# Optimization experiments

Measured on AMD Instinct MI355X. Metric: run time of the kernel, lower is better.

Reference implementation:

```python
import jax, jax.numpy as jnp
import numpy as np
import math

DN = ('NCHW', 'OIHW', 'NCHW')

def conv(x, w, b, stride=1, pad=0):
    y = jax.lax.conv_general_dilated(x, w, (stride, stride), ((pad, pad), (pad, pad)), dimension_numbers=DN)
    return y + b[None, :, None, None]

def conv_t(x, w, b, stride=2, k=4, p=1):
    # torch ConvTranspose2d: weight (Cin, Cout, kH, kW). Equivalent fractionally-strided conv:
    w2 = jnp.transpose(w[:, :, ::-1, ::-1], (1, 0, 2, 3))  # -> (Cout, Cin, kH, kW), spatially flipped
    pp = k - 1 - p
    y = jax.lax.conv_general_dilated(x, w2, (1, 1), ((pp, pp), (pp, pp)), lhs_dilation=(stride, stride), dimension_numbers=DN)
    return y + b[None, :, None, None]

def res_stack(h, w1, b1, w2, b2):
    # w1: [L, rh, nh, 3, 3], w2: [L, nh, rh, 1, 1]
    for i in range(w1.shape[0]):
        t = conv(jax.nn.relu(h), w1[i], b1[i], 1, 1)
        t = conv(jax.nn.relu(t), w2[i], b2[i], 1, 0)
        h = h + t
    return jax.nn.relu(h)

def setup_inputs() -> dict:
    key = jax.random.key(0)
    ks = jax.random.split(key, 16)
    D, K = 64, 512
    limit = math.sqrt(3.0 / D)
    def w(k, shape, scale=0.05):
        return (jax.random.normal(k, shape, dtype=jnp.float32) * scale)
    return {
        'x': jax.random.normal(ks[0], (16, 3, 256, 256), dtype=jnp.float32),
        'enc_w0': w(ks[1], (64, 3, 4, 4)), 'enc_b0': jnp.zeros((64,), jnp.float32),
        'enc_w1': w(ks[2], (128, 64, 4, 4)), 'enc_b1': jnp.zeros((128,), jnp.float32),
        'enc_wf': w(ks[3], (128, 128, 3, 3)), 'enc_bf': jnp.zeros((128,), jnp.float32),
        'enc_res_w1': w(ks[4], (2, 32, 128, 3, 3)), 'enc_res_b1': jnp.zeros((2, 32), jnp.float32),
        'enc_res_w2': w(ks[5], (2, 128, 32, 1, 1)), 'enc_res_b2': jnp.zeros((2, 128), jnp.float32),
        'pre_w': w(ks[6], (64, 128, 1, 1)), 'pre_b': jnp.zeros((64,), jnp.float32),
        'codebook': jax.random.uniform(ks[7], (D, K), jnp.float32, -limit, limit),
        'dec_w': w(ks[8], (128, 64, 3, 3)), 'dec_b': jnp.zeros((128,), jnp.float32),
        'dec_res_w1': w(ks[9], (2, 32, 128, 3, 3)), 'dec_res_b1': jnp.zeros((2, 32), jnp.float32),
        'dec_res_w2': w(ks[10], (2, 128, 32, 1, 1)), 'dec_res_b2': jnp.zeros((2, 128), jnp.float32),
        'up_w0': w(ks[11], (128, 64, 4, 4)), 'up_b0': jnp.zeros((64,), jnp.float32),
        'up_w1': w(ks[12], (64, 3, 4, 4)), 'up_b1': jnp.zeros((3,), jnp.float32),
    }

def reference(x, enc_w0, enc_b0, enc_w1, enc_b1, enc_wf, enc_bf,
              enc_res_w1, enc_res_b1, enc_res_w2, enc_res_b2,
              pre_w, pre_b, codebook,
              dec_w, dec_b, dec_res_w1, dec_res_b1, dec_res_w2, dec_res_b2,
              up_w0, up_b0, up_w1, up_b1):
    # --- Encoder ---
    h = jax.nn.relu(conv(x, enc_w0, enc_b0, 2, 1))
    h = jax.nn.relu(conv(h, enc_w1, enc_b1, 2, 1))
    h = conv(h, enc_wf, enc_bf, 1, 1)
    h = res_stack(h, enc_res_w1, enc_res_b1, enc_res_w2, enc_res_b2)
    z = conv(h, pre_w, pre_b, 1, 0)  # [B, 64, 64, 64]
    # --- Vector quantizer (cdist + argmin + gather, straight-through) ---
    B, D, H, W = z.shape
    flat = jnp.transpose(z, (0, 2, 3, 1)).reshape(-1, D)  # [BHW, D]
    dist = (flat ** 2).sum(1, keepdims=True) - 2.0 * (flat @ codebook) + (codebook ** 2).sum(0)[None, :]
    idx = jnp.argmin(dist, axis=1)  # [BHW]
    q = codebook.T[idx].reshape(B, H, W, D).transpose(0, 3, 1, 2)
    zq = z + jax.lax.stop_gradient(q - z)  # straight-through estimator
    # --- Decoder ---
    h = conv(zq, dec_w, dec_b, 1, 1)
    h = res_stack(h, dec_res_w1, dec_res_b1, dec_res_w2, dec_res_b2)
    h = jax.nn.relu(conv_t(h, up_w0, up_b0, 2, 4, 1))
    x_recon = conv_t(h, up_w1, up_b1, 2, 4, 1)
    return x_recon
```

## Files before the change

### kernel.cpp

```cpp
#include <hip/hip_runtime.h>
#include <math.h>


#define DEV __device__ __forceinline__

DEV int rfl(int v) { return __builtin_amdgcn_readfirstlane(v); }

DEV void async_copy16(const float* g, float* l) {
  __builtin_amdgcn_global_load_lds(
      (const __attribute__((address_space(1))) void*)g,
      (__attribute__((address_space(3))) void*)l, 16, 0, 0);
}

typedef __attribute__((ext_vector_type(8))) _Float16 h16x8;
typedef __attribute__((ext_vector_type(4))) float f32x4;

DEV ushort f2h(float f) {
  _Float16 h = (_Float16)f;
  return __builtin_bit_cast(ushort, h);
}
DEV float h2f(ushort u) { return (float)__builtin_bit_cast(_Float16, u); }
DEV uint pk(ushort a, ushort b) { return (uint)a | ((uint)b << 16); }

template<int CIN, int COT>
__global__ __launch_bounds__(256) void prep_w3s(
    const float* __restrict__ w, ushort* __restrict__ wpk) {
  constexpr int nCh = CIN / 32, nM = COT / 16;
  const int t = blockIdx.x * 256 + threadIdx.x;
  if (t >= 9 * nCh * nM * 64) return;
  const int l = t & 63;
  const int m = (t >> 6) % nM;
  const int sid = t / (64 * nM);
  const int ch = sid / 9, khkw = sid % 9;
  const int co = m * 16 + (l & 15);
  const int k8 = (l >> 4) * 8;
  const int sw = (16 * l) ^ ((l & 4) ? 8 : 0);
  ushort* slab = wpk + (size_t)sid * (nM * 1024) + m * 1024;
#pragma unroll
  for (int i = 0; i < 8; i++) {
    const int ci = ch * 32 + k8 + i;
    const float v = w[((size_t)co * CIN + ci) * 9 + khkw];
    const ushort hi = f2h(v);
    slab[sw + i]       = hi;
    slab[(sw ^ 8) + i] = f2h((v - h2f(hi)) * 2048.0f);
  }
}

template<int CIN, int COT>
__global__ __launch_bounds__(256) void prep_w4s(
    const float* __restrict__ w, ushort* __restrict__ wpk) {
  const int t = blockIdx.x * 256 + threadIdx.x;
  if (t >= 16384) return;
  const int l = t & 63;
  const int m = (t >> 6) & 7;
  const int sid = t >> 9;
  const int step = sid >> 3, rr = (sid >> 2) & 1, kw = sid & 3;
  const int ch = step >> 1, h = step & 1;
  const int kh = 2 * h + rr;
  const int tap = kh * 4 + kw;
  const int co = m * 16 + (l & 15);
  const int k8 = (l >> 4) * 8;
  const int sw = (16 * l) ^ ((l & 4) ? 8 : 0);
  ushort* slab = wpk + (size_t)sid * 8192 + m * 1024;
#pragma unroll
  for (int i = 0; i < 8; i++) {
    const int ci = ch * 32 + k8 + i;
    const float v = w[((size_t)co * CIN + ci) * 16 + tap];
    const ushort hi = f2h(v);
    slab[sw + i]       = hi;
    slab[(sw ^ 8) + i] = f2h((v - h2f(hi)) * 2048.0f);
  }
}

template<int CIN, int COT>
__global__ __launch_bounds__(256) void prep_wts(
    const float* __restrict__ w, ushort* __restrict__ wpk) {
  constexpr int nCh = CIN / 32, nM = COT / 16;
  const int t = blockIdx.x * 256 + threadIdx.x;
  if (t >= 16 * nCh * nM * 64) return;
  const int l = t & 63;
  const int m = (t >> 6) % nM;
  const int sid = t / (64 * nM);
  const int ch = sid >> 4, idx = sid & 15;
  const int ord[16] = {15, 13, 14, 12, 7, 11, 5, 6, 9, 10, 4, 8, 3, 1, 2, 0};
  const int tap = ord[idx];
  const int kh = tap >> 2, kw = tap & 3;
  const int co = m * 16 + (l & 15);
  const int k8 = (l >> 4) * 8;
  const int sw = (16 * l) ^ ((l & 4) ? 8 : 0);
  ushort* slab = wpk + (size_t)sid * (nM * 1024) + m * 1024;
#pragma unroll
  for (int i = 0; i < 8; i++) {
    const int ci = ch * 32 + k8 + i;
    const float v = w[(((size_t)ci * COT + co) * 4 + kh) * 4 + kw];
    const ushort hi = f2h(v);
    slab[sw + i]       = hi;
    slab[(sw ^ 8) + i] = f2h((v - h2f(hi)) * 2048.0f);
  }
}

__global__ __launch_bounds__(256) void prep_cb(
    const float* __restrict__ cb, ushort* __restrict__ cbpk) {
  const int t = blockIdx.x * 256 + threadIdx.x;
  const int l = t & 63;
  const int m = (t >> 6) & 31;
  const int c = t >> 11;
  const int entry = m * 16 + (l & 15);
  ushort* o = cbpk + (size_t)t * 16;
#pragma unroll
  for (int i = 0; i < 8; i++) {
    const int d = c * 32 + (l >> 4) * 8 + i;
    const float v = cb[d * 512 + entry];
    const ushort hi = f2h(v);
    o[i]     = hi;
    o[8 + i] = f2h((v - h2f(hi)) * 2048.0f);
  }
}

__global__ __launch_bounds__(256) void cvt_cbn(
    const float* __restrict__ cb, float* __restrict__ cbn) {
  const int k = blockIdx.x * 256 + threadIdx.x;
  if (k >= 512) return;
  double s = 0.0;
  for (int d = 0; d < 64; d++) {
    const double c = (double)cb[d * 512 + k];
    s = fma(c, c, s);
  }
  cbn[k] = (float)s;
}

__global__ __launch_bounds__(256) void vq_mfma(
    const float* __restrict__ cb, const ushort* __restrict__ cbpk,
    const float* __restrict__ cbn, float* __restrict__ zq) {
  const int tid = threadIdx.x;
  const int l = tid & 63;
  const int w = rfl(tid >> 6);
  const int n = blockIdx.x >> 6, row = blockIdx.x & 63;
  float* zp = zq + (size_t)n * 262144 + row * 64;
  const int pos = w * 16 + (l & 15);

  h16x8 zh[2], zl[2];
#pragma unroll
  for (int c = 0; c < 2; c++) {
#pragma unroll
    for (int i = 0; i < 8; i++) {
      const int d = c * 32 + (l >> 4) * 8 + i;
      const float v = zp[(size_t)d * 4096 + pos];
      const _Float16 h = (_Float16)v;
      zh[c][i] = h;
      zl[c][i] = (_Float16)((v - (float)h) * 2048.0f);
    }
  }

  const float SCL = 1.0f / 2048.0f;
  float bestd = 1e30f;
  int best = 0;
  for (int grp = 0; grp < 4; grp++) {
    f32x4 aH[8], aM[8];
#pragma unroll
    for (int m = 0; m < 8; m++) {
      aH[m] = (f32x4){0.f, 0.f, 0.f, 0.f};
      aM[m] = (f32x4){0.f, 0.f, 0.f, 0.f};
    }
#pragma unroll
    for (int c = 0; c < 2; c++) {
#pragma unroll
      for (int m = 0; m < 8; m++) {
        const ushort* ap = cbpk + ((size_t)(c * 32 + grp * 8 + m) * 64 + l) * 16;
        const h16x8 ah = *(const h16x8*)ap;
        const h16x8 al = *(const h16x8*)(ap + 8);
        aH[m] = __builtin_amdgcn_mfma_f32_16x16x32_f16(ah, zh[c], aH[m], 0, 0, 0);
        aM[m] = __builtin_amdgcn_mfma_f32_16x16x32_f16(al, zh[c], aM[m], 0, 0, 0);
        aM[m] = __builtin_amdgcn_mfma_f32_16x16x32_f16(ah, zl[c], aM[m], 0, 0, 0);
      }
    }
#pragma unroll
    for (int m = 0; m < 8; m++) {
#pragma unroll
      for (int j = 0; j < 4; j++) {
        const int k = grp * 128 + m * 16 + ((l >> 4) << 2) + j;
        const float dd = aH[m][j] + aM[m][j] * SCL;
        const float dist = fmaf(-2.0f, dd, cbn[k]);
        if (dist < bestd) { bestd = dist; best = k; }
      }
    }
  }

#pragma unroll
  for (int off = 16; off <= 32; off <<= 1) {
    const float d2 = __shfl_xor(bestd, off, 64);
    const int i2 = __shfl_xor(best, off, 64);
    if (d2 < bestd || (d2 == bestd && i2 < best)) { bestd = d2; best = i2; }
  }

#pragma unroll
  for (int i = 0; i < 16; i++) {
    const int d = (l >> 4) * 16 + i;
    zp[(size_t)d * 4096 + pos] = cb[d * 512 + best];
  }
}

template<int CIN, int COT, bool RELU_OUT>
__global__ __launch_bounds__(256, 2) void conv4s2_mfma(
    const float* __restrict__ x, const ushort* __restrict__ wpk,
    const float* __restrict__ bias, float* __restrict__ y) {
  constexpr int nCh = CIN / 32, nM = COT / 16;
  constexpr int nStep = nCh * 2;
  constexpr int nTap = nStep * 8;
  __shared__ ushort act[2][2][2][66][40];
  __shared__ ushort wlds[2][8192];
  const int tid = threadIdx.x;
  const int l = tid & 63;
  const int wv = rfl(tid >> 6);
  const int ho = (blockIdx.x & 7) * 8 + (blockIdx.x >> 3);
  const int n = blockIdx.z;

  {
    uint* lp = (uint*)&act[0][0][0][0][0];
    for (int s = tid; s < 16 * 20; s += 256) {
      const int c = s / 20, w32 = s % 20;
      const int which = c & 1, rest = c >> 1;
      lp[(size_t)(rest * 66 + (which ? 65 : 0)) * 20 + w32] = 0;
    }
  }

  const float* xn = x + ((size_t)n * CIN) * 16384;

  float2 sreg[2][4][2];
  float rmask[2];
  auto LOADG = [&](int step) {
    const int ch = step >> 1, h = step & 1;
#pragma unroll
    for (int rr = 0; rr < 2; rr++) {
      const int ir = 2 * ho - 1 + 2 * h + rr;
      const bool ok = (ir >= 0) && (ir < 128);
      const int irc = ok ? ir : 0;
      rmask[rr] = ok ? 1.0f : 0.0f;
#pragma unroll
      for (int cc = 0; cc < 4; cc++) {
        const int ci0 = ch * 32 + cc * 8 + wv * 2;
        sreg[rr][cc][0] = *(const float2*)(xn + (size_t)ci0 * 16384 + irc * 128 + 2 * l);
        sreg[rr][cc][1] = *(const float2*)(xn + (size_t)(ci0 + 1) * 16384 + irc * 128 + 2 * l);
      }
    }
  };
  auto WRITE = [&]() {
    uint* base = (uint*)&act[0][0][0][0][0];
#pragma unroll
    for (int rr = 0; rr < 2; rr++) {
#pragma unroll
      for (int cc = 0; cc < 4; cc++) {
        const float e0 = sreg[rr][cc][0].x * rmask[rr], o0 = sreg[rr][cc][0].y * rmask[rr];
        const float e1 = sreg[rr][cc][1].x * rmask[rr], o1 = sreg[rr][cc][1].y * rmask[rr];
        const ushort he0 = f2h(e0), ho_0 = f2h(o0);
        const ushort he1 = f2h(e1), ho_1 = f2h(o1);
        const ushort le0 = f2h((e0 - h2f(he0)) * 2048.0f);
        const ushort lo0 = f2h((o0 - h2f(ho_0)) * 2048.0f);
        const ushort le1 = f2h((e1 - h2f(he1)) * 2048.0f);
        const ushort lo1 = f2h((o1 - h2f(ho_1)) * 2048.0f);
        const int u = cc * 4 + wv;
        const size_t sl20 = (size_t)(l + 1) * 20 + u;
        base[(size_t)((0 * 2 + rr) * 2 + 0) * 1320 + sl20] = pk(he0, he1);
        base[(size_t)((0 * 2 + rr) * 2 + 1) * 1320 + sl20] = pk(ho_0, ho_1);
        base[(size_t)((1 * 2 + rr) * 2 + 0) * 1320 + sl20] = pk(le0, le1);
        base[(size_t)((1 * 2 + rr) * 2 + 1) * 1320 + sl20] = pk(lo0, lo1);
      }
    }
  };
  auto STAGEW = [&](int t, int buf) {
    const ushort* src = wpk + (size_t)t * 8192;
    ushort* dst = &wlds[buf][0];
#pragma unroll
    for (int j = 0; j < 4; j++)
      async_copy16((const float*)(src + (j * 256 + tid) * 8),
                   (float*)(dst + (j * 256 + tid) * 8));
  };

  f32x4 accH[nM], accM[nM];
#pragma unroll
  for (int m = 0; m < nM; m++) {
    const int co = m * 16 + ((l >> 4) << 2);
    accH[m] = (f32x4){bias[co], bias[co + 1], bias[co + 2], bias[co + 3]};
    accM[m] = (f32x4){0.f, 0.f, 0.f, 0.f};
  }

  const int pb = wv * 16;
  const int sw = (16 * l) ^ ((l & 4) ? 8 : 0);
  STAGEW(0, 0);
  LOADG(0);
  int tcnt = 0;
  for (int step = 0; step < nStep; step++) {
    __syncthreads();
    WRITE();
    __syncthreads();
#pragma unroll
    for (int rr = 0; rr < 2; rr++) {
#pragma unroll
      for (int kw = 0; kw < 4; kw++) {
        if (!(rr == 0 && kw == 0)) __syncthreads();
        if (tcnt + 1 < nTap) STAGEW(tcnt + 1, (tcnt + 1) & 1);
        if (rr == 0 && kw == 0 && step + 1 < nStep) LOADG(step + 1);
        const ushort* wb = &wlds[tcnt & 1][0];
        const int eo = (kw == 0 || kw == 2) ? 1 : 0;
        const int sh = (kw == 0) ? 0 : (kw == 3) ? 2 : 1;
        const int sl = pb + (l & 15) + sh;
        const h16x8 bh = *(const h16x8*)(&act[0][rr][eo][sl][(l >> 4) * 8]);
        const h16x8 bl = *(const h16x8*)(&act[1][rr][eo][sl][(l >> 4) * 8]);
#pragma unroll
        for (int m = 0; m < nM; m++) {
          const h16x8 ah = *(const h16x8*)(wb + m * 1024 + sw);
          const h16x8 al = *(const h16x8*)(wb + m * 1024 + (sw ^ 8));
          accH[m] = __builtin_amdgcn_mfma_f32_16x16x32_f16(ah, bh, accH[m], 0, 0, 0);
          accM[m] = __builtin_amdgcn_mfma_f32_16x16x32_f16(al, bh, accM[m], 0, 0, 0);
          accM[m] = __builtin_amdgcn_mfma_f32_16x16x32_f16(ah, bl, accM[m], 0, 0, 0);
        }
        tcnt++;
      }
    }
  }

  const float SCL = 1.0f / 2048.0f;
  const int pos = pb + (l & 15);
  const int r4 = (l >> 4) << 2;
#pragma unroll
  for (int m = 0; m < nM; m++) {
    const int co = m * 16 + r4;
    float* yp = y + (((size_t)(n * COT + co)) * 64 + ho) * 64 + pos;
#pragma unroll
    for (int j = 0; j < 4; j++) {
      float v = accH[m][j] + accM[m][j] * SCL;
      if (RELU_OUT) v = fmaxf(v, 0.f);
      yp[(size_t)j * 4096] = v;
    }
  }
}

template<int CIN, int COT, bool RELU_IN>
__global__ __launch_bounds__(256, 2) void conv3_mfma(
    const float* __restrict__ x, const ushort* __restrict__ wpk,
    const float* __restrict__ bias, float* __restrict__ y) {
  constexpr int nCh = CIN / 32, nM = COT / 16;
  constexpr int nTap = nCh * 9;
  __shared__ ushort act[2][3 * 66 * 40];
  __shared__ ushort wlds[2][nM * 1024];
  const int tid = threadIdx.x;
  const int l = tid & 63;
  const int wv = rfl(tid >> 6);
  const int r = blockIdx.x;
  const int n = blockIdx.z;

  {
    uint* lp = (uint*)&act[0][0];
    for (int s = tid; s < 12 * 20; s += 256) {
      const int c = s / 20, w32 = s % 20;
      const int which = c & 1;
      const int rowrel = (c >> 1) % 3;
      const int plane  = (c >> 1) / 3;
      lp[(size_t)(plane * 198 + rowrel * 66 + (which ? 65 : 0)) * 20 + w32] = 0;
    }
  }

  const float* xn = x + ((size_t)n * CIN) * 4096;

  float sreg[3][4][2];
  auto LOADG = [&](int ch) {
#pragma unroll
    for (int rr = 0; rr < 3; rr++) {
      const int ir = r - 1 + rr;
      const bool ok = (ir >= 0) && (ir < 64);
#pragma unroll
      for (int cc = 0; cc < 4; cc++) {
        const int ci0 = ch * 32 + cc * 8 + wv * 2;
        sreg[rr][cc][0] = ok ? xn[((size_t)ci0 * 64 + ir) * 64 + l] : 0.f;
        sreg[rr][cc][1] = ok ? xn[((size_t)(ci0 + 1) * 64 + ir) * 64 + l] : 0.f;
      }
    }
  };
  auto WRITE = [&]() {
    uint* ph = (uint*)&act[0][0];
    uint* pl = (uint*)&act[1][0];
#pragma unroll
    for (int rr = 0; rr < 3; rr++) {
#pragma unroll
      for (int cc = 0; cc < 4; cc++) {
        float v0 = sreg[rr][cc][0], v1 = sreg[rr][cc][1];
        if (RELU_IN) { v0 = fmaxf(v0, 0.f); v1 = fmaxf(v1, 0.f); }
        const ushort h0 = f2h(v0), h1 = f2h(v1);
        const ushort m0 = f2h((v0 - h2f(h0)) * 2048.0f);
        const ushort m1 = f2h((v1 - h2f(h1)) * 2048.0f);
        const int idx = (rr * 66 + (l + 1)) * 20 + cc * 4 + wv;
        ph[idx] = (uint)h0 | ((uint)h1 << 16);
        pl[idx] = (uint)m0 | ((uint)m1 << 16);
      }
    }
  };
  auto STAGEW = [&](int t, int buf) {
    const ushort* src = wpk + (size_t)t * (nM * 1024);
    ushort* dst = &wlds[buf][0];
#pragma unroll
    for (int j = 0; j < nM / 2; j++)
      async_copy16((const float*)(src + (j * 256 + tid) * 8),
                   (float*)(dst + (j * 256 + tid) * 8));
  };

  f32x4 accH[nM], accM[nM];
#pragma unroll
  for (int m = 0; m < nM; m++) {
    const int co = m * 16 + ((l >> 4) << 2);
    accH[m] = (f32x4){bias[co], bias[co + 1], bias[co + 2], bias[co + 3]};
    accM[m] = (f32x4){0.f, 0.f, 0.f, 0.f};
  }

  const int pb = wv * 16;
  const int sw = (16 * l) ^ ((l & 4) ? 8 : 0);
  STAGEW(0, 0);
  LOADG(0);
  int tcnt = 0;
  for (int ch = 0; ch < nCh; ch++) {
    __syncthreads();
    WRITE();
    __syncthreads();
#pragma unroll
    for (int kh = 0; kh < 3; kh++) {
#pragma unroll
      for (int kw = 0; kw < 3; kw++) {
        if (!(kh == 0 && kw == 0)) __syncthreads();
        if (tcnt + 1 < nTap) STAGEW(tcnt + 1, (tcnt + 1) & 1);
        if (kh == 0 && kw == 0 && ch + 1 < nCh) LOADG(ch + 1);
        const ushort* wb = &wlds[tcnt & 1][0];
        const int slot = kh * 66 + pb + (l & 15) + kw;
        const h16x8 bh = *(const h16x8*)(&act[0][0] + slot * 40 + (l >> 4) * 8);
        const h16x8 bl = *(const h16x8*)(&act[1][0] + slot * 40 + (l >> 4) * 8);
#pragma unroll
        for (int m = 0; m < nM; m++) {
          const h16x8 ah = *(const h16x8*)(wb + m * 1024 + sw);
          const h16x8 al = *(const h16x8*)(wb + m * 1024 + (sw ^ 8));
          accH[m] = __builtin_amdgcn_mfma_f32_16x16x32_f16(ah, bh, accH[m], 0, 0, 0);
          accM[m] = __builtin_amdgcn_mfma_f32_16x16x32_f16(al, bh, accM[m], 0, 0, 0);
          accM[m] = __builtin_amdgcn_mfma_f32_16x16x32_f16(ah, bl, accM[m], 0, 0, 0);
        }
        tcnt++;
      }
    }
  }

  const float SCL = 1.0f / 2048.0f;
  const int pos = pb + (l & 15);
  const int r4 = (l >> 4) << 2;
#pragma unroll
  for (int m = 0; m < nM; m++) {
    const int co = m * 16 + r4;
    float* yp = y + (((size_t)(n * COT + co)) * 64 + r) * 64 + pos;
#pragma unroll
    for (int j = 0; j < 4; j++)
      yp[(size_t)j * 4096] = accH[m][j] + accM[m][j] * SCL;
  }
}

template<int CIN, int COT, bool RELU_OUT>
__global__ __launch_bounds__(256, 2) void convt_mfma(
    const float* __restrict__ x, const ushort* __restrict__ wpk,
    const float* __restrict__ bias, float* __restrict__ y) {
  constexpr int nCh = CIN / 32, nM = COT / 16;
  constexpr int nPair = nCh * 8;
  __shared__ ushort act[2][3 * 66 * 40];
  __shared__ ushort wlds[2][2 * nM * 1024];
  const int tid = threadIdx.x;
  const int l = tid & 63;
  const int wv = rfl(tid >> 6);
  const int a = blockIdx.x;
  const int n = blockIdx.z;

  {
    uint* lp = (uint*)&act[0][0];
    for (int s = tid; s < 12 * 20; s += 256) {
      const int c = s / 20, w32 = s % 20;
      const int which = c & 1;
      const int rowrel = (c >> 1) % 3;
      const int plane  = (c >> 1) / 3;
      lp[(size_t)(plane * 198 + rowrel * 66 + (which ? 65 : 0)) * 20 + w32] = 0;
    }
  }

  const float* xn = x + ((size_t)n * CIN) * 4096;

  float sreg[3][4][2];
  auto LOADG = [&](int ch) {
#pragma unroll
    for (int rr = 0; rr < 3; rr++) {
      const int ir = a - 1 + rr;
      const bool ok = (ir >= 0) && (ir < 64);
#pragma unroll
      for (int cc = 0; cc < 4; cc++) {
        const int ci0 = ch * 32 + cc * 8 + wv * 2;
        sreg[rr][cc][0] = ok ? xn[((size_t)ci0 * 64 + ir) * 64 + l] : 0.f;
        sreg[rr][cc][1] = ok ? xn[((size_t)(ci0 + 1) * 64 + ir) * 64 + l] : 0.f;
      }
    }
  };
  auto WRITE = [&]() {
    uint* ph = (uint*)&act[0][0];
    uint* pl = (uint*)&act[1][0];
#pragma unroll
    for (int rr = 0; rr < 3; rr++) {
#pragma unroll
      for (int cc = 0; cc < 4; cc++) {
        const float v0 = sreg[rr][cc][0], v1 = sreg[rr][cc][1];
        const ushort h0 = f2h(v0), h1 = f2h(v1);
        const ushort m0 = f2h((v0 - h2f(h0)) * 2048.0f);
        const ushort m1 = f2h((v1 - h2f(h1)) * 2048.0f);
        const int idx = (rr * 66 + (l + 1)) * 20 + cc * 4 + wv;
        ph[idx] = (uint)h0 | ((uint)h1 << 16);
        pl[idx] = (uint)m0 | ((uint)m1 << 16);
      }
    }
  };
  auto STAGEW2 = [&](int p, int buf) {
    const ushort* src = wpk + (size_t)p * (2 * nM * 1024);
    ushort* dst = &wlds[buf][0];
#pragma unroll
    for (int j = 0; j < nM; j++)
      async_copy16((const float*)(src + (j * 256 + tid) * 8),
                   (float*)(dst + (j * 256 + tid) * 8));
  };

  f32x4 aH[4][nM], aM[4][nM];
#pragma unroll
  for (int m = 0; m < nM; m++) {
    const int co = m * 16 + ((l >> 4) << 2);
    const f32x4 b4 = (f32x4){bias[co], bias[co + 1], bias[co + 2], bias[co + 3]};
#pragma unroll
    for (int o = 0; o < 4; o++) { aH[o][m] = b4; aM[o][m] = (f32x4){0.f,0.f,0.f,0.f}; }
  }

  const int pb = wv * 16;
  const int sw = (16 * l) ^ ((l & 4) ? 8 : 0);
  STAGEW2(0, 0);
  LOADG(0);
  int pcnt = 0;

#define CT_TAP(WOFS, RR, DD, OIDX) {                                          \
    const int slot = (RR) * 66 + pb + (l & 15) + 1 + (DD);                    \
    const h16x8 bh = *(const h16x8*)(&act[0][0] + slot * 40 + (l >> 4) * 8);  \
    const h16x8 bl = *(const h16x8*)(&act[1][0] + slot * 40 + (l >> 4) * 8);  \
    _Pragma("unroll")                                                         \
    for (int m = 0; m < nM; m++) {                                            \
      const h16x8 ah = *(const h16x8*)(wb + (WOFS) + m * 1024 + sw);          \
      const h16x8 al = *(const h16x8*)(wb + (WOFS) + m * 1024 + (sw ^ 8));    \
      aH[OIDX][m] = __builtin_amdgcn_mfma_f32_16x16x32_f16(ah, bh, aH[OIDX][m], 0, 0, 0); \
      aM[OIDX][m] = __builtin_amdgcn_mfma_f32_16x16x32_f16(al, bh, aM[OIDX][m], 0, 0, 0); \
      aM[OIDX][m] = __builtin_amdgcn_mfma_f32_16x16x32_f16(ah, bl, aM[OIDX][m], 0, 0, 0); \
    }}
#define CT_PHASE(RRA, DDA, OA, RRB, DDB, OB) {                                \
    if (!first) __syncthreads();                                              \
    first = false;                                                            \
    if (pcnt + 1 < nPair) STAGEW2(pcnt + 1, (pcnt + 1) & 1);                  \
    if (doLoad) { if (ch + 1 < nCh) LOADG(ch + 1); doLoad = false; }          \
    const ushort* wb = &wlds[pcnt & 1][0];                                    \
    CT_TAP(0, RRA, DDA, OA)                                                   \
    CT_TAP(nM * 1024, RRB, DDB, OB)                                           \
    pcnt++; }

  for (int ch = 0; ch < nCh; ch++) {
    __syncthreads();
    WRITE();
    __syncthreads();
    bool first = true, doLoad = true;
    CT_PHASE(0, -1, 0,  0,  0, 0)
    CT_PHASE(0,  0, 1,  0, +1, 1)
    CT_PHASE(1, -1, 0,  1, -1, 2)
    CT_PHASE(1,  0, 0,  1,  0, 1)
    CT_PHASE(1,  0, 2,  1,  0, 3)
    CT_PHASE(1, +1, 1,  1, +1, 3)
    CT_PHASE(2, -1, 2,  2,  0, 2)
    CT_PHASE(2,  0, 3,  2, +1, 3)
  }
#undef CT_TAP
#undef CT_PHASE

  const float SCL = 1.0f / 2048.0f;
  const int b = pb + (l & 15);
  const int oh0 = 2 * a;
  const int r4 = (l >> 4) << 2;
#pragma unroll
  for (int m = 0; m < nM; m++) {
    const int co = m * 16 + r4;
#pragma unroll
    for (int j = 0; j < 4; j++) {
      float v0e = aH[0][m][j] + aM[0][m][j] * SCL;
      float v0o = aH[1][m][j] + aM[1][m][j] * SCL;
      float v1e = aH[2][m][j] + aM[2][m][j] * SCL;
      float v1o = aH[3][m][j] + aM[3][m][j] * SCL;
      if (RELU_OUT) {
        v0e = fmaxf(v0e, 0.f); v0o = fmaxf(v0o, 0.f);
        v1e = fmaxf(v1e, 0.f); v1o = fmaxf(v1o, 0.f);
      }
      float* row0 = y + (((size_t)(n * COT + co + j)) * 128 + oh0) * 128;
      ((float2*)row0)[b] = make_float2(v0e, v0o);
      ((float2*)(row0 + 128))[b] = make_float2(v1e, v1o);
    }
  }
}

template<int CIN, int COT, bool RELU_OUT, int OW>
__global__ __launch_bounds__(256) void conv4s2_row(
    const float* __restrict__ x, const float* __restrict__ w,
    const float* __restrict__ bias, float* __restrict__ y,
    int Hout, int Cout) {
  const int Win = OW * 2, Hin = Hout * 2;
  const int t = blockIdx.x * 256 + threadIdx.x;
  const int wo = t & (OW - 1);
  const int ho = rfl(t / OW);
  const int co0 = blockIdx.y * COT, n = blockIdx.z;

  float acc[COT];
#pragma unroll
  for (int u = 0; u < COT; u++) acc[u] = bias[co0 + u];

  const int iw0 = 2 * wo - 1;
  const int cA = iw0 < 0 ? 0 : iw0;
  const bool mA = iw0 >= 0;
  const int cD = (iw0 + 3 < Win) ? iw0 + 3 : Win - 1;
  const bool mD = iw0 + 3 < Win;

  for (int ci = 0; ci < CIN; ci++) {
    const float* xp = x + ((size_t)(n * CIN + ci)) * Hin * Win;
    const float* wp = w + ((size_t)(co0 * CIN + ci)) * 16;
#pragma unroll
    for (int kh = 0; kh < 4; kh++) {
      const int ih = 2 * ho - 1 + kh;
      if (ih >= 0 && ih < Hin) {
        const float* row = xp + (size_t)ih * Win;
        float x0 = row[cA];      x0 = mA ? x0 : 0.f;
        float x1 = row[iw0 + 1];
        float x2 = row[iw0 + 2];
        float x3 = row[cD];      x3 = mD ? x3 : 0.f;
#pragma unroll
        for (int u = 0; u < COT; u++) {
          const float* wr = wp + u * CIN * 16 + kh * 4;
          acc[u] = fmaf(x0, wr[0], acc[u]);
          acc[u] = fmaf(x1, wr[1], acc[u]);
          acc[u] = fmaf(x2, wr[2], acc[u]);
          acc[u] = fmaf(x3, wr[3], acc[u]);
        }
      }
    }
  }
#pragma unroll
  for (int u = 0; u < COT; u++) {
    float v = acc[u];
    if (RELU_OUT) v = fmaxf(v, 0.f);
    y[(((size_t)(n * Cout + co0 + u)) * Hout + ho) * OW + wo] = v;
  }
}

template<int CIN, int COT, bool RELU_IN, bool ACCUM, bool RELU_OUT>
__global__ __launch_bounds__(256) void conv1x1_v4(
    const float* __restrict__ x, const float* __restrict__ w,
    const float* __restrict__ bias, float* __restrict__ y,
    int HW, int Cout) {
  const int p = (blockIdx.x * 256 + threadIdx.x) * 4;
  const int co0 = blockIdx.y * COT, n = blockIdx.z;

  float4 acc[COT];
#pragma unroll
  for (int u = 0; u < COT; u++) {
    const float b = bias[co0 + u];
    acc[u] = make_float4(b, b, b, b);
  }
  for (int ci = 0; ci < CIN; ci++) {
    float4 xv = *(const float4*)&x[((size_t)(n * CIN + ci)) * HW + p];
    if (RELU_IN) {
      xv.x = fmaxf(xv.x, 0.f); xv.y = fmaxf(xv.y, 0.f);
      xv.z = fmaxf(xv.z, 0.f); xv.w = fmaxf(xv.w, 0.f);
    }
#pragma unroll
    for (int u = 0; u < COT; u++) {
      const float wv = w[(co0 + u) * CIN + ci];
      acc[u].x = fmaf(xv.x, wv, acc[u].x);
      acc[u].y = fmaf(xv.y, wv, acc[u].y);
      acc[u].z = fmaf(xv.z, wv, acc[u].z);
      acc[u].w = fmaf(xv.w, wv, acc[u].w);
    }
  }
#pragma unroll
  for (int u = 0; u < COT; u++) {
    float4* yp = (float4*)&y[((size_t)(n * Cout + co0 + u)) * HW + p];
    float4 r = acc[u];
    if (ACCUM) {
      float4 h = *yp;
      r.x += h.x; r.y += h.y; r.z += h.z; r.w += h.w;
    }
    if (RELU_OUT) {
      r.x = fmaxf(r.x, 0.f); r.y = fmaxf(r.y, 0.f);
      r.z = fmaxf(r.z, 0.f); r.w = fmaxf(r.w, 0.f);
    }
    *yp = r;
  }
}

template<int CIN, int COT, bool RELU_IN, bool RELU_OUT, int WH>
__global__ __launch_bounds__(256) void convt_row(
    const float* __restrict__ x, const float* __restrict__ w,
    const float* __restrict__ bias, float* __restrict__ y,
    int Hin, int Cout) {
  const int Hout = Hin * 2;
  const int t = blockIdx.x * 256 + threadIdx.x;
  const int a = t & (WH - 1);
  const int oh = rfl(t / WH);
  const int co0 = blockIdx.y * COT, n = blockIdx.z;

  float acc0[COT], acc1[COT];
#pragma unroll
  for (int u = 0; u < COT; u++) { acc0[u] = bias[co0 + u]; acc1[u] = bias[co0 + u]; }

  const int cm = a > 0 ? a - 1 : 0;
  const bool mm = a > 0;
  const int cp = a < WH - 1 ? a + 1 : WH - 1;
  const bool mp = a < WH - 1;

  const int kh0 = (oh + 1) & 1;
#pragma unroll
  for (int dh = 0; dh < 2; dh++) {
    const int kh = kh0 + 2 * dh;
    const int ih = (oh + 1 - kh) >> 1;
    if (ih >= 0 && ih < Hin) {
      for (int ci = 0; ci < CIN; ci++) {
        const float* row = x + (((size_t)(n * CIN + ci)) * Hin + ih) * WH;
        float x0  = row[a];
        float xm1 = row[cm];  xm1 = mm ? xm1 : 0.f;
        float xp1 = row[cp];  xp1 = mp ? xp1 : 0.f;
        if (RELU_IN) {
          x0 = fmaxf(x0, 0.f); xm1 = fmaxf(xm1, 0.f); xp1 = fmaxf(xp1, 0.f);
        }
        const float* wp = w + ((size_t)(ci * Cout + co0)) * 16 + kh * 4;
#pragma unroll
        for (int u = 0; u < COT; u++) {
          const float* wr = wp + u * 16;
          acc0[u] = fmaf(x0,  wr[1], acc0[u]);
          acc0[u] = fmaf(xm1, wr[3], acc0[u]);
          acc1[u] = fmaf(xp1, wr[0], acc1[u]);
          acc1[u] = fmaf(x0,  wr[2], acc1[u]);
        }
      }
    }
  }
#pragma unroll
  for (int u = 0; u < COT; u++) {
    float v0 = acc0[u], v1 = acc1[u];
    if (RELU_OUT) { v0 = fmaxf(v0, 0.f); v1 = fmaxf(v1, 0.f); }
    float* row = y + (((size_t)(n * Cout + co0 + u)) * Hout + oh) * (2 * WH);
    ((float2*)row)[a] = make_float2(v0, v1);
  }
}

extern "C" void kernel_launch(void* const* d_in, const int* in_sizes, int n_in,
                              void* d_out, int out_size, void* d_ws, size_t ws_size,
                              hipStream_t stream) {
  const float* x          = (const float*)d_in[0];
  const float* enc_w0     = (const float*)d_in[1];
  const float* enc_b0     = (const float*)d_in[2];
  const float* enc_w1     = (const float*)d_in[3];
  const float* enc_b1     = (const float*)d_in[4];
  const float* enc_wf     = (const float*)d_in[5];
  const float* enc_bf     = (const float*)d_in[6];
  const float* enc_res_w1 = (const float*)d_in[7];
  const float* enc_res_b1 = (const float*)d_in[8];
  const float* enc_res_w2 = (const float*)d_in[9];
  const float* enc_res_b2 = (const float*)d_in[10];
  const float* pre_w      = (const float*)d_in[11];
  const float* pre_b      = (const float*)d_in[12];
  const float* codebook   = (const float*)d_in[13];
  const float* dec_w      = (const float*)d_in[14];
  const float* dec_b      = (const float*)d_in[15];
  const float* dec_res_w1 = (const float*)d_in[16];
  const float* dec_res_b1 = (const float*)d_in[17];
  const float* dec_res_w2 = (const float*)d_in[18];
  const float* dec_res_b2 = (const float*)d_in[19];
  const float* up_w0      = (const float*)d_in[20];
  const float* up_b0      = (const float*)d_in[21];
  const float* up_w1      = (const float*)d_in[22];
  const float* up_b1      = (const float*)d_in[23];
  float* out = (float*)d_out;

  float* A = (float*)d_ws;
  float* B = A + 16777216;
  float* C = B + 8388608;
  ushort* wpkF  = (ushort*)(A + 8388608);
  ushort* wpkEa = wpkF  + 294912;
  ushort* wpkEb = wpkEa + 73728;
  ushort* wpkD  = wpkEb + 73728;
  ushort* wpkDa = wpkD  + 147456;
  ushort* wpkDb = wpkDa + 73728;
  ushort* cbpk  = wpkDb + 73728;
  float*  cbn   = (float*)(cbpk + 131072);
  ushort* wpk1  = (ushort*)C;
  ushort* wpkT  = wpk1 + 262144;

  const dim3 blk(256);
  const int N = 16;

  prep_w4s<64, 128><<<dim3(64), blk, 0, stream>>>(enc_w1, wpk1);

  conv4s2_row<3, 16, true, 128><<<dim3(64, 4, N), blk, 0, stream>>>(
      x, enc_w0, enc_b0, A, 128, 64);
  conv4s2_mfma<64, 128, true><<<dim3(64, 1, N), blk, 0, stream>>>(
      A, wpk1, enc_b1, B);

  prep_w3s<128, 128><<<dim3(72), blk, 0, stream>>>(enc_wf, wpkF);
  prep_w3s<128, 32><<<dim3(18), blk, 0, stream>>>(enc_res_w1, wpkEa);
  prep_w3s<128, 32><<<dim3(18), blk, 0, stream>>>(
      enc_res_w1 + (size_t)32 * 128 * 9, wpkEb);
  prep_w3s<64, 128><<<dim3(36), blk, 0, stream>>>(dec_w, wpkD);
  prep_w3s<128, 32><<<dim3(18), blk, 0, stream>>>(dec_res_w1, wpkDa);
  prep_w3s<128, 32><<<dim3(18), blk, 0, stream>>>(
      dec_res_w1 + (size_t)32 * 128 * 9, wpkDb);
  prep_cb<<<dim3(16), blk, 0, stream>>>(codebook, cbpk);
  cvt_cbn<<<dim3(2), blk, 0, stream>>>(codebook, cbn);

  conv3_mfma<128, 128, false><<<dim3(64, 1, N), blk, 0, stream>>>(
      B, wpkF, enc_bf, C);
  conv3_mfma<128, 32, true><<<dim3(64, 1, N), blk, 0, stream>>>(
      C, wpkEa, enc_res_b1, A);
  conv1x1_v4<32, 8, true, true, false><<<dim3(4, 16, N), blk, 0, stream>>>(
      A, enc_res_w2, enc_res_b2, C, 4096, 128);
  conv3_mfma<128, 32, true><<<dim3(64, 1, N), blk, 0, stream>>>(
      C, wpkEb, enc_res_b1 + 32, A);
  conv1x1_v4<32, 8, true, true, true><<<dim3(4, 16, N), blk, 0, stream>>>(
      A, enc_res_w2 + (size_t)128 * 32, enc_res_b2 + 128, C, 4096, 128);
  conv1x1_v4<128, 8, false, false, false><<<dim3(4, 8, N), blk, 0, stream>>>(
      C, pre_w, pre_b, A, 4096, 64);

  prep_wts<128, 64><<<dim3(64), blk, 0, stream>>>(up_w0, wpkT);

  vq_mfma<<<dim3(1024), blk, 0, stream>>>(codebook, cbpk, cbn, A);

  conv3_mfma<64, 128, false><<<dim3(64, 1, N), blk, 0, stream>>>(
      A, wpkD, dec_b, B);
  conv3_mfma<128, 32, true><<<dim3(64, 1, N), blk, 0, stream>>>(
      B, wpkDa, dec_res_b1, A);
  conv1x1_v4<32, 8, true, true, false><<<dim3(4, 16, N), blk, 0, stream>>>(
      A, dec_res_w2, dec_res_b2, B, 4096, 128);
  conv3_mfma<128, 32, true><<<dim3(64, 1, N), blk, 0, stream>>>(
      B, wpkDb, dec_res_b1 + 32, A);
  conv1x1_v4<32, 8, true, true, true><<<dim3(4, 16, N), blk, 0, stream>>>(
      A, dec_res_w2 + (size_t)128 * 32, dec_res_b2 + 128, B, 4096, 128);
  convt_mfma<128, 64, true><<<dim3(64, 1, N), blk, 0, stream>>>(
      B, wpkT, up_b0, A);
  convt_row<64, 3, false, false, 128><<<dim3(128, 1, N), blk, 0, stream>>>(
      A, up_w1, up_b1, out, 128, 3);
}
```

Before: 762.9 us.

## Compute two output rows per block in 3x3 MFMA conv to reuse weights

The 3x3 convolution kernel now computes two adjacent output rows per block instead of one. It stages four input rows in LDS and keeps two sets of accumulators, so each weight fragment loaded from LDS feeds twice as many MFMAs, and weight staging and sync overhead are halved per output. The grid is halved to 32 row-pairs per image, which lowers block count and parallelism. Register pressure rises, with 128-channel outputs needing 16 f32x4 accumulators per lane, and LDS use grows.

```diff
diff --git a/kernel.cpp b/kernel.cpp
--- a/kernel.cpp
+++ b/kernel.cpp
@@ -336,37 +336,37 @@
 }
 
 template<int CIN, int COT, bool RELU_IN>
-__global__ __launch_bounds__(256, 2) void conv3_mfma(
+__global__ __launch_bounds__(256, 2) void conv3_mfma2(
     const float* __restrict__ x, const ushort* __restrict__ wpk,
     const float* __restrict__ bias, float* __restrict__ y) {
   constexpr int nCh = CIN / 32, nM = COT / 16;
   constexpr int nTap = nCh * 9;
-  __shared__ ushort act[2][3 * 66 * 40];
+  __shared__ ushort act[2][4 * 66 * 40];
   __shared__ ushort wlds[2][nM * 1024];
   const int tid = threadIdx.x;
   const int l = tid & 63;
   const int wv = rfl(tid >> 6);
-  const int r = blockIdx.x;
+  const int r0 = blockIdx.x * 2;
   const int n = blockIdx.z;
 
   {
     uint* lp = (uint*)&act[0][0];
-    for (int s = tid; s < 12 * 20; s += 256) {
+    for (int s = tid; s < 16 * 20; s += 256) {
       const int c = s / 20, w32 = s % 20;
       const int which = c & 1;
-      const int rowrel = (c >> 1) % 3;
-      const int plane  = (c >> 1) / 3;
-      lp[(size_t)(plane * 198 + rowrel * 66 + (which ? 65 : 0)) * 20 + w32] = 0;
+      const int rowrel = (c >> 1) & 3;
+      const int plane  = c >> 3;
+      lp[(size_t)(plane * 264 + rowrel * 66 + (which ? 65 : 0)) * 20 + w32] = 0;
     }
   }
 
   const float* xn = x + ((size_t)n * CIN) * 4096;
 
-  float sreg[3][4][2];
+  float sreg[4][4][2];
   auto LOADG = [&](int ch) {
 #pragma unroll
-    for (int rr = 0; rr < 3; rr++) {
-      const int ir = r - 1 + rr;
+    for (int rr = 0; rr < 4; rr++) {
+      const int ir = r0 - 1 + rr;
       const bool ok = (ir >= 0) && (ir < 64);
 #pragma unroll
       for (int cc = 0; cc < 4; cc++) {
@@ -380,7 +380,7 @@
     uint* ph = (uint*)&act[0][0];
     uint* pl = (uint*)&act[1][0];
 #pragma unroll
-    for (int rr = 0; rr < 3; rr++) {
+    for (int rr = 0; rr < 4; rr++) {
 #pragma unroll
       for (int cc = 0; cc < 4; cc++) {
         float v0 = sreg[rr][cc][0], v1 = sreg[rr][cc][1];
@@ -403,12 +403,16 @@
                    (float*)(dst + (j * 256 + tid) * 8));
   };
 
-  f32x4 accH[nM], accM[nM];
+  f32x4 accH[2][nM], accM[2][nM];
 #pragma unroll
   for (int m = 0; m < nM; m++) {
     const int co = m * 16 + ((l >> 4) << 2);
-    accH[m] = (f32x4){bias[co], bias[co + 1], bias[co + 2], bias[co + 3]};
-    accM[m] = (f32x4){0.f, 0.f, 0.f, 0.f};
+    const f32x4 b4 = (f32x4){bias[co], bias[co + 1], bias[co + 2], bias[co + 3]};
+#pragma unroll
+    for (int ro = 0; ro < 2; ro++) {
+      accH[ro][m] = b4;
+      accM[ro][m] = (f32x4){0.f, 0.f, 0.f, 0.f};
+    }
   }
 
   const int pb = wv * 16;
@@ -428,16 +432,23 @@
         if (tcnt + 1 < nTap) STAGEW(tcnt + 1, (tcnt + 1) & 1);
         if (kh == 0 && kw == 0 && ch + 1 < nCh) LOADG(ch + 1);
         const ushort* wb = &wlds[tcnt & 1][0];
-        const int slot = kh * 66 + pb + (l & 15) + kw;
-        const h16x8 bh = *(const h16x8*)(&act[0][0] + slot * 40 + (l >> 4) * 8);
-        const h16x8 bl = *(const h16x8*)(&act[1][0] + slot * 40 + (l >> 4) * 8);
+        h16x8 bh[2], bl[2];
+#pragma unroll
+        for (int ro = 0; ro < 2; ro++) {
+          const int slot = (ro + kh) * 66 + pb + (l & 15) + kw;
+          bh[ro] = *(const h16x8*)(&act[0][0] + slot * 40 + (l >> 4) * 8);
+          bl[ro] = *(const h16x8*)(&act[1][0] + slot * 40 + (l >> 4) * 8);
+        }
 #pragma unroll
         for (int m = 0; m < nM; m++) {
           const h16x8 ah = *(const h16x8*)(wb + m * 1024 + sw);
           const h16x8 al = *(const h16x8*)(wb + m * 1024 + (sw ^ 8));
-          accH[m] = __builtin_amdgcn_mfma_f32_16x16x32_f16(ah, bh, accH[m], 0, 0, 0);
-          accM[m] = __builtin_amdgcn_mfma_f32_16x16x32_f16(al, bh, accM[m], 0, 0, 0);
-          accM[m] = __builtin_amdgcn_mfma_f32_16x16x32_f16(ah, bl, accM[m], 0, 0, 0);
+#pragma unroll
+          for (int ro = 0; ro < 2; ro++) {
+            accH[ro][m] = __builtin_amdgcn_mfma_f32_16x16x32_f16(ah, bh[ro], accH[ro][m], 0, 0, 0);
+            accM[ro][m] = __builtin_amdgcn_mfma_f32_16x16x32_f16(al, bh[ro], accM[ro][m], 0, 0, 0);
+            accM[ro][m] = __builtin_amdgcn_mfma_f32_16x16x32_f16(ah, bl[ro], accM[ro][m], 0, 0, 0);
+          }
         }
         tcnt++;
       }
@@ -448,12 +459,15 @@
   const int pos = pb + (l & 15);
   const int r4 = (l >> 4) << 2;
 #pragma unroll
-  for (int m = 0; m < nM; m++) {
-    const int co = m * 16 + r4;
-    float* yp = y + (((size_t)(n * COT + co)) * 64 + r) * 64 + pos;
-#pragma unroll
-    for (int j = 0; j < 4; j++)
-      yp[(size_t)j * 4096] = accH[m][j] + accM[m][j] * SCL;
+  for (int ro = 0; ro < 2; ro++) {
+#pragma unroll
+    for (int m = 0; m < nM; m++) {
+      const int co = m * 16 + r4;
+      float* yp = y + (((size_t)(n * COT + co)) * 64 + (r0 + ro)) * 64 + pos;
+#pragma unroll
+      for (int j = 0; j < 4; j++)
+        yp[(size_t)j * 4096] = accH[ro][m][j] + accM[ro][m][j] * SCL;
+    }
   }
 }
 
@@ -818,13 +832,13 @@
   prep_cb<<<dim3(16), blk, 0, stream>>>(codebook, cbpk);
   cvt_cbn<<<dim3(2), blk, 0, stream>>>(codebook, cbn);
 
-  conv3_mfma<128, 128, false><<<dim3(64, 1, N), blk, 0, stream>>>(
+  conv3_mfma2<128, 128, false><<<dim3(32, 1, N), blk, 0, stream>>>(
       B, wpkF, enc_bf, C);
-  conv3_mfma<128, 32, true><<<dim3(64, 1, N), blk, 0, stream>>>(
+  conv3_mfma2<128, 32, true><<<dim3(32, 1, N), blk, 0, stream>>>(
       C, wpkEa, enc_res_b1, A);
   conv1x1_v4<32, 8, true, true, false><<<dim3(4, 16, N), blk, 0, stream>>>(
       A, enc_res_w2, enc_res_b2, C, 4096, 128);
-  conv3_mfma<128, 32, true><<<dim3(64, 1, N), blk, 0, stream>>>(
+  conv3_mfma2<128, 32, true><<<dim3(32, 1, N), blk, 0, stream>>>(
       C, wpkEb, enc_res_b1 + 32, A);
   conv1x1_v4<32, 8, true, true, true><<<dim3(4, 16, N), blk, 0, stream>>>(
       A, enc_res_w2 + (size_t)128 * 32, enc_res_b2 + 128, C, 4096, 128);
@@ -835,13 +849,13 @@
 
   vq_mfma<<<dim3(1024), blk, 0, stream>>>(codebook, cbpk, cbn, A);
 
-  conv3_mfma<64, 128, false><<<dim3(64, 1, N), blk, 0, stream>>>(
+  conv3_mfma2<64, 128, false><<<dim3(32, 1, N), blk, 0, stream>>>(
       A, wpkD, dec_b, B);
-  conv3_mfma<128, 32, true><<<dim3(64, 1, N), blk, 0, stream>>>(
+  conv3_mfma2<128, 32, true><<<dim3(32, 1, N), blk, 0, stream>>>(
       B, wpkDa, dec_res_b1, A);
   conv1x1_v4<32, 8, true, true, false><<<dim3(4, 16, N), blk, 0, stream>>>(
       A, dec_res_w2, dec_res_b2, B, 4096, 128);
-  conv3_mfma<128, 32, true><<<dim3(64, 1, N), blk, 0, stream>>>(
+  conv3_mfma2<128, 32, true><<<dim3(32, 1, N), blk, 0, stream>>>(
       B, wpkDb, dec_res_b1 + 32, A);
   conv1x1_v4<32, 8, true, true, true><<<dim3(4, 16, N), blk, 0, stream>>>(
       A, dec_res_w2 + (size_t)128 * 32, dec_res_b2 + 128, B, 4096, 128);
```

New measurement: 790.0 us. 3.6% more time.
